# Optimization experiments

Hardware: AMD Instinct MI355X
Metric: run time of the kernel (lower is better)

## Reference

```python
import jax, jax.numpy as jnp
import numpy as np

BLOCK = (4, 8, 8)   # (t, h, w)
NH, D, DA = 8, 512, 64
EPS = 1e-5


def _layernorm(x, g, b):
    m = jnp.mean(x, axis=-1, keepdims=True)
    xc = x - m
    v = jnp.mean(xc * xc, axis=-1, keepdims=True)
    return xc * jax.lax.rsqrt(v + EPS) * g + b


def setup_inputs() -> dict:
    key = jax.random.key(0)
    ks = jax.random.split(key, 10)
    B, T, H, W = 2, 8, 32, 32
    t, h, w = BLOCK
    s_qkv = (2.0 / (D + DA)) ** 0.5   # xavier_normal for (d, da) fan
    s_lin = (2.0 / (D + D)) ** 0.5
    return {
        "x": jax.random.normal(ks[0], (B, D, T, H, W), jnp.float32),
        "dt_bank": 0.02 * jax.random.normal(ks[1], (NH, 2 * t - 1), jnp.float32),
        "dh_bank": 0.02 * jax.random.normal(ks[2], (NH, 2 * h - 1), jnp.float32),
        "dw_bank": 0.02 * jax.random.normal(ks[3], (NH, 2 * w - 1), jnp.float32),
        "ln1_g": jnp.ones((D,), jnp.float32),
        "ln1_b": jnp.zeros((D,), jnp.float32),
        "w_q": s_qkv * jax.random.normal(ks[4], (NH, D, DA), jnp.float32),
        "w_k": s_qkv * jax.random.normal(ks[5], (NH, D, DA), jnp.float32),
        "w_v": s_qkv * jax.random.normal(ks[6], (NH, D, DA), jnp.float32),
        "w_proj": s_lin * jax.random.normal(ks[7], (D, NH * DA), jnp.float32),
        "ln2_g": jnp.ones((D,), jnp.float32),
        "ln2_b": jnp.zeros((D,), jnp.float32),
        "w1": s_lin * jax.random.normal(ks[8], (D, D), jnp.float32),
        "b1": jnp.zeros((D,), jnp.float32),
        "w2": s_lin * jax.random.normal(ks[9], (D, D), jnp.float32),
        "b2": jnp.zeros((D,), jnp.float32),
    }


def _axial_bias(dt_bank, dh_bank, dw_bank):
    t, h, w = BLOCK
    thw = t * h * w
    ar = jnp.arange(thw)
    tt = ar // (h * w)
    hh = (ar // w) % h
    ww = ar % w
    # relative offsets shifted to be non-negative (matches dt += abs(dt.min()))
    it = tt[:, None] - tt[None, :] + (t - 1)
    ih = hh[:, None] - hh[None, :] + (h - 1)
    iw = ww[:, None] - ww[None, :] + (w - 1)
    return dt_bank[:, it] + dh_bank[:, ih] + dw_bank[:, iw]  # (NH, thw, thw)


def reference(x, dt_bank, dh_bank, dw_bank, ln1_g, ln1_b, w_q, w_k, w_v,
              w_proj, ln2_g, ln2_b, w1, b1, w2, b2):
    B, C, T, H, W = x.shape
    t, h, w = BLOCK
    st, sh, sw = T // t, H // h, W // w
    thw = t * h * w
    nb = B * st * sh * sw

    # block split: (B,C,T,H,W) -> (nb, thw, C)
    xb = x.reshape(B, C, st, t, sh, h, sw, w).transpose(0, 2, 4, 6, 1, 3, 5, 7)
    xb = xb.reshape(nb, C, thw).transpose(0, 2, 1)

    Bb = _axial_bias(dt_bank, dh_bank, dw_bank)  # (NH, thw, thw)

    # --- multi-head attention with additive axial bias ---
    resid = xb
    xn = _layernorm(xb, ln1_g, ln1_b)
    q = jnp.einsum('bnd,hde->hbne', xn, w_q)
    k = jnp.einsum('bnd,hde->hbne', xn, w_k)
    v = jnp.einsum('bnd,hde->hbne', xn, w_v)
    scale = 1.0 / jnp.sqrt(jnp.asarray(DA, x.dtype))
    attn = jnp.einsum('hbne,hbme->hbnm', q, k) * scale + Bb[:, None]
    attn = jax.nn.softmax(attn, axis=-1)
    out = jnp.einsum('hbnm,hbme->hbne', attn, v)         # (NH, nb, thw, DA)
    out = out.transpose(1, 2, 0, 3).reshape(nb, thw, NH * DA)  # head-major concat
    out = out @ w_proj.T + resid

    # --- FFN with residual ---
    y = _layernorm(out, ln2_g, ln2_b)
    y = jax.nn.relu(y @ w1.T + b1) @ w2.T + b2
    out = y + out

    # un-block: (nb, thw, C) -> (B,C,T,H,W)
    out = out.transpose(0, 2, 1).reshape(B, st, sh, sw, C, t, h, w)
    out = out.transpose(0, 4, 1, 5, 2, 6, 3, 7).reshape(B, C, T, H, W)
    return out
```

## Files before the change

kernel.cpp:

```cpp
#include <hip/hip_runtime.h>
#include <hip/hip_bf16.h>
#include <stdint.h>

typedef __attribute__((ext_vector_type(4))) float f32x4;
typedef __attribute__((ext_vector_type(8))) short s16x8;
typedef __attribute__((ext_vector_type(4))) short s16x4;
typedef __attribute__((ext_vector_type(8))) __bf16 b16x8;

__device__ __forceinline__ f32x4 mfma16(s16x8 a, s16x8 b, f32x4 c) {
  return __builtin_amdgcn_mfma_f32_16x16x32_bf16(
      __builtin_bit_cast(b16x8, a), __builtin_bit_cast(b16x8, b), c, 0, 0, 0);
}

__device__ __forceinline__ void gl_lds16(const void* g, void* l) {
  __builtin_amdgcn_global_load_lds(
      (const __attribute__((address_space(1))) void*)g,
      (__attribute__((address_space(3))) void*)l, 16, 0, 0);
}

__device__ __forceinline__ unsigned short f2bf(float f) {
  union { float f; unsigned u; } v; v.f = f;
  unsigned u = v.u;
  return (unsigned short)((u + 0x7FFFu + ((u >> 16) & 1u)) >> 16);
}

__global__ __launch_bounds__(256) void k_prep(
    const float* __restrict__ wq, const float* __restrict__ wk, const float* __restrict__ wv,
    const float* __restrict__ wp, const float* __restrict__ w1, const float* __restrict__ w2,
    unsigned short* __restrict__ qkvT, unsigned short* __restrict__ wpT,
    unsigned short* __restrict__ w1T, unsigned short* __restrict__ w2T)
{
  int i = blockIdx.x * 256 + threadIdx.x;
  if (i < 786432) {
    int n = i >> 9, d = i & 511;
    const float* src = (n < 512) ? wq : (n < 1024 ? wk : wv);
    int nn = n & 511;
    int h = nn >> 6, e = nn & 63;
    qkvT[i] = f2bf(src[((size_t)h * 512 + d) * 64 + e]);
  } else {
    int j = i - 786432;
    int w = j >> 18;
    int o = j & 262143;
    const float* s = (w == 0) ? wp : (w == 1 ? w1 : w2);
    unsigned short* dst = (w == 0) ? wpT : (w == 1 ? w1T : w2T);
    dst[o] = f2bf(s[o]);
  }
}

__global__ __launch_bounds__(256) void k_gather_ln(
    const float* __restrict__ x, const float* __restrict__ g1, const float* __restrict__ b1,
    float* __restrict__ xb, unsigned short* __restrict__ xn)
{
  __shared__ float lx[16][517];
  int gid = blockIdx.x;
  int h2 = gid & 1, hh = (gid >> 1) & 7, tt = (gid >> 4) & 3,
      shI = (gid >> 6) & 3, stI = (gid >> 8) & 1, bI = (gid >> 9) & 1;
  const float* xbase = x + (size_t)bI * 4194304 + (size_t)(stI * 4 + tt) * 1024
                       + (shI * 8 + hh) * 32 + h2 * 16;
  int t = threadIdx.x;
  for (int i = 0; i < 8; ++i) {
    int slot = i * 256 + t;
    int c = slot >> 2, w8 = slot & 3;
    const float4 v = *(const float4*)(xbase + (size_t)c * 8192 + w8 * 4);
    lx[w8 * 4 + 0][c] = v.x; lx[w8 * 4 + 1][c] = v.y;
    lx[w8 * 4 + 2][c] = v.z; lx[w8 * 4 + 3][c] = v.w;
  }
  __syncthreads();
  int lane = t & 63, wid = t >> 6;
  for (int q = 0; q < 4; ++q) {
    int widx = wid * 4 + q;
    float vv[8]; float s = 0.f, ss = 0.f;
    #pragma unroll
    for (int i = 0; i < 8; ++i) { float v = lx[widx][lane + i * 64]; vv[i] = v; s += v; ss += v * v; }
    #pragma unroll
    for (int d = 1; d < 64; d <<= 1) { s += __shfl_xor(s, d); ss += __shfl_xor(ss, d); }
    float mean = s * (1.f / 512.f);
    float var = ss * (1.f / 512.f) - mean * mean;
    float rs = rsqrtf(var + 1e-5f);
    int sw = h2 * 2 + (widx >> 3), ww = widx & 7;
    int blk = ((bI * 2 + stI) * 4 + shI) * 4 + sw;
    int n = tt * 64 + hh * 8 + ww;
    size_t base = ((size_t)blk * 256 + n) * 512;
    #pragma unroll
    for (int i = 0; i < 8; ++i) {
      int c = lane + i * 64;
      float v = vv[i];
      xb[base + c] = v;
      xn[base + c] = f2bf((v - mean) * rs * g1[c] + b1[c]);
    }
  }
}

template<int EPI>
__global__ __launch_bounds__(256, 2) void k_gemm(
    const unsigned short* __restrict__ A, const unsigned short* __restrict__ Bt,
    int M, int N,
    unsigned short* __restrict__ Cbf, float* __restrict__ Cf,
    const float* __restrict__ bias, const float* __restrict__ addf,
    unsigned short* __restrict__ vTout)
{
  constexpr int K = 512;
  __shared__ __align__(16) unsigned short a_lds[128 * 64];
  __shared__ __align__(16) unsigned short b_lds[128 * 64];
  int tid = threadIdx.x, lane = tid & 63, wid = tid >> 6;
  int m0 = blockIdx.x * 128, n0 = blockIdx.y * 128;
  int wm = (wid >> 1) * 64, wn = (wid & 1) * 64;
  int r15 = lane & 15, g = lane >> 4;

  f32x4 acc[4][4] = {};

  for (int ks = 0; ks < K; ks += 64) {
    #pragma unroll
    for (int s = 0; s < 4; ++s) {
      int seg = wid * 4 + s;
      int slot = seg * 64 + lane;
      int m = slot >> 3, lc = (slot & 7) ^ (m & 7);
      gl_lds16(A + (size_t)(m0 + m) * K + ks + lc * 8, (char*)a_lds + seg * 1024);
      gl_lds16(Bt + (size_t)(n0 + m) * K + ks + lc * 8, (char*)b_lds + seg * 1024);
    }
    __syncthreads();
    #pragma unroll
    for (int kk = 0; kk < 2; ++kk) {
      s16x8 af[4], bfr[4];
      #pragma unroll
      for (int f = 0; f < 4; ++f) {
        int mm = wm + f * 16 + r15;
        af[f] = *(const s16x8*)((const char*)a_lds + mm * 128 + (((kk * 4 + g) ^ (mm & 7)) * 16));
        int nn = wn + f * 16 + r15;
        bfr[f] = *(const s16x8*)((const char*)b_lds + nn * 128 + (((kk * 4 + g) ^ (nn & 7)) * 16));
      }
      #pragma unroll
      for (int fm = 0; fm < 4; ++fm)
        #pragma unroll
        for (int fn = 0; fn < 4; ++fn)
          acc[fm][fn] = mfma16(af[fm], bfr[fn], acc[fm][fn]);
    }
    __syncthreads();
  }

  int g4 = g * 4;
  #pragma unroll
  for (int fm = 0; fm < 4; ++fm) {
    #pragma unroll
    for (int fn = 0; fn < 4; ++fn) {
      int col = n0 + wn + fn * 16 + r15;
      int row0 = m0 + wm + fm * 16 + g4;
      if (EPI == 0 && col >= 1024) {
        int h = (col - 1024) >> 6, e = col & 63;
        int blk = row0 >> 8, mtok = row0 & 255;
        s16x4 pk;
        #pragma unroll
        for (int r = 0; r < 4; ++r) pk[r] = (short)f2bf(acc[fm][fn][r]);
        *(s16x4*)(vTout + (((size_t)blk * 8 + h) * 64 + e) * 256 + mtok) = pk;
      } else {
        #pragma unroll
        for (int r = 0; r < 4; ++r) {
          int row = row0 + r;
          float v = acc[fm][fn][r];
          if (EPI == 0) {
            Cbf[(size_t)row * 1536 + col] = f2bf(v);
          } else if (EPI == 1) {
            Cf[(size_t)row * 512 + col] = v + addf[(size_t)row * 512 + col];
          } else if (EPI == 2) {
            Cbf[(size_t)row * 512 + col] = f2bf(fmaxf(v + bias[col], 0.f));
          } else {
            Cf[(size_t)row * 512 + col] = v + bias[col] + addf[(size_t)row * 512 + col];
          }
        }
      }
    }
  }
}

__global__ __launch_bounds__(256, 2) void k_attn(
    const unsigned short* __restrict__ qkv, const unsigned short* __restrict__ vT,
    const float* __restrict__ dtb, const float* __restrict__ dhb, const float* __restrict__ dwb,
    unsigned short* __restrict__ aout)
{
  __shared__ __align__(16) unsigned short k_lds[64 * 64];
  __shared__ __align__(16) unsigned short v_lds[64 * 64];
  __shared__ __align__(16) unsigned short p_lds[4][64 * 64];
  __shared__ float bt_s[7], bh_s[15], bw_s[15];

  int tid = threadIdx.x, lane = tid & 63, wid = tid >> 6;
  int bk = blockIdx.x >> 3, h = blockIdx.x & 7;
  if (tid < 7) bt_s[tid] = dtb[h * 7 + tid];
  else if (tid < 22) bh_s[tid - 7] = dhb[h * 15 + tid - 7];
  else if (tid < 37) bw_s[tid - 22] = dwb[h * 15 + tid - 22];

  int r15 = lane & 15, g = lane >> 4;
  int wq0 = wid * 64;

  s16x8 qf[4][2];
  #pragma unroll
  for (int fn = 0; fn < 4; ++fn)
    #pragma unroll
    for (int kk = 0; kk < 2; ++kk)
      qf[fn][kk] = *(const s16x8*)(qkv + (size_t)(bk * 256 + wq0 + fn * 16 + r15) * 1536
                                   + h * 64 + kk * 32 + g * 8);

  f32x4 o[4][4] = {};
  float mrun[4] = {-1e30f, -1e30f, -1e30f, -1e30f};
  float lrun[4] = {0.f, 0.f, 0.f, 0.f};

  for (int mt = 0; mt < 4; ++mt) {
    int m0 = mt * 64;
    #pragma unroll
    for (int s = 0; s < 4; ++s) {
      int sg = wid * 4 + s;
      if (sg < 8) {
        int slot = sg * 64 + lane;
        int m = slot >> 3, lc = (slot & 7) ^ (m & 7);
        gl_lds16(qkv + (size_t)(bk * 256 + m0 + m) * 1536 + 512 + h * 64 + lc * 8,
                 (char*)k_lds + sg * 1024);
      } else {
        int slot = (sg - 8) * 64 + lane;
        int e = slot >> 3, lc = (slot & 7) ^ (e & 7);
        gl_lds16(vT + (((size_t)bk * 8 + h) * 64 + e) * 256 + m0 + lc * 8,
                 (char*)v_lds + (sg - 8) * 1024);
      }
    }
    __syncthreads();

    f32x4 st[4][4] = {};
    #pragma unroll
    for (int kk = 0; kk < 2; ++kk) {
      s16x8 kf[4];
      #pragma unroll
      for (int fm = 0; fm < 4; ++fm) {
        int m = fm * 16 + r15;
        kf[fm] = *(const s16x8*)((const char*)k_lds + m * 128 + (((kk * 4 + g) ^ (m & 7)) * 16));
      }
      #pragma unroll
      for (int fm = 0; fm < 4; ++fm)
        #pragma unroll
        for (int fn = 0; fn < 4; ++fn)
          st[fm][fn] = mfma16(kf[fm], qf[fn][kk], st[fm][fn]);
    }

    #pragma unroll
    for (int fn = 0; fn < 4; ++fn) {
      int n = wq0 + fn * 16 + r15;
      int ttn = n >> 6, hhn = (n >> 3) & 7, wwn = n & 7;
      float btc = bt_s[ttn - mt + 3];
      float bwv[4];
      #pragma unroll
      for (int r = 0; r < 4; ++r) bwv[r] = bw_s[wwn - (4 * (g & 1) + r) + 7];
      float vals[16];
      float mx = -1e30f;
      #pragma unroll
      for (int fm = 0; fm < 4; ++fm) {
        float bhv = bh_s[hhn - (fm * 2 + (g >> 1)) + 7];
        #pragma unroll
        for (int r = 0; r < 4; ++r) {
          float v = st[fm][fn][r] * 0.125f + btc + bhv + bwv[r];
          vals[fm * 4 + r] = v;
          mx = fmaxf(mx, v);
        }
      }
      mx = fmaxf(mx, __shfl_xor(mx, 16));
      mx = fmaxf(mx, __shfl_xor(mx, 32));
      float mnew = fmaxf(mrun[fn], mx);
      float alpha = __expf(mrun[fn] - mnew);
      mrun[fn] = mnew;
      float sum = 0.f;
      #pragma unroll
      for (int fm = 0; fm < 4; ++fm) {
        s16x4 pk;
        #pragma unroll
        for (int r = 0; r < 4; ++r) {
          float p = __expf(vals[fm * 4 + r] - mnew);
          sum += p;
          pk[r] = (short)f2bf(p);
        }
        int lc = fm * 2 + (g >> 1);
        int nl = fn * 16 + r15;
        *(s16x4*)((char*)(&p_lds[wid][0]) + nl * 128 + ((lc ^ (nl & 7)) * 16) + (g & 1) * 8) = pk;
      }
      sum += __shfl_xor(sum, 16);
      sum += __shfl_xor(sum, 32);
      lrun[fn] = lrun[fn] * alpha + sum;
      #pragma unroll
      for (int fe = 0; fe < 4; ++fe)
        #pragma unroll
        for (int r = 0; r < 4; ++r)
          o[fe][fn][r] *= alpha;
    }
    asm volatile("s_waitcnt lgkmcnt(0)" ::: "memory");

    #pragma unroll
    for (int mm = 0; mm < 2; ++mm) {
      s16x8 vf[4], pf[4];
      #pragma unroll
      for (int fe = 0; fe < 4; ++fe) {
        int e = fe * 16 + r15;
        vf[fe] = *(const s16x8*)((const char*)v_lds + e * 128 + (((mm * 4 + g) ^ (e & 7)) * 16));
      }
      #pragma unroll
      for (int fn = 0; fn < 4; ++fn) {
        int nl = fn * 16 + r15;
        pf[fn] = *(const s16x8*)((const char*)(&p_lds[wid][0]) + nl * 128 + (((mm * 4 + g) ^ (nl & 7)) * 16));
      }
      #pragma unroll
      for (int fe = 0; fe < 4; ++fe)
        #pragma unroll
        for (int fn = 0; fn < 4; ++fn)
          o[fe][fn] = mfma16(vf[fe], pf[fn], o[fe][fn]);
    }
    __syncthreads();
  }

  #pragma unroll
  for (int fn = 0; fn < 4; ++fn) {
    float inv = 1.f / lrun[fn];
    #pragma unroll
    for (int fe = 0; fe < 4; ++fe)
      #pragma unroll
      for (int r = 0; r < 4; ++r)
        o[fe][fn][r] *= inv;
  }
  #pragma unroll
  for (int fe = 0; fe < 4; ++fe) {
    int lc = fe * 2 + (g >> 1);
    #pragma unroll
    for (int fn = 0; fn < 4; ++fn) {
      int nl = fn * 16 + r15;
      s16x4 pk;
      #pragma unroll
      for (int r = 0; r < 4; ++r) pk[r] = (short)f2bf(o[fe][fn][r]);
      *(s16x4*)((char*)(&p_lds[wid][0]) + nl * 128 + ((lc ^ (nl & 7)) * 16) + (g & 1) * 8) = pk;
    }
  }
  asm volatile("s_waitcnt lgkmcnt(0)" ::: "memory");
  #pragma unroll
  for (int it = 0; it < 8; ++it) {
    int nl = it * 8 + (lane >> 3);
    int lc = lane & 7;
    s16x8 v = *(const s16x8*)((const char*)(&p_lds[wid][0]) + nl * 128 + ((lc ^ (nl & 7)) * 16));
    *(s16x8*)(aout + (size_t)(bk * 256 + wq0 + nl) * 512 + h * 64 + lc * 8) = v;
  }
}

__global__ __launch_bounds__(256) void k_ln2(
    const float* __restrict__ in, const float* __restrict__ g2, const float* __restrict__ b2,
    unsigned short* __restrict__ out)
{
  int token = blockIdx.x * 4 + (threadIdx.x >> 6);
  int lane = threadIdx.x & 63;
  const float* row = in + (size_t)token * 512;
  float vv[8]; float s = 0.f, ss = 0.f;
  #pragma unroll
  for (int i = 0; i < 8; ++i) { float v = row[lane + i * 64]; vv[i] = v; s += v; ss += v * v; }
  #pragma unroll
  for (int d = 1; d < 64; d <<= 1) { s += __shfl_xor(s, d); ss += __shfl_xor(ss, d); }
  float mean = s * (1.f / 512.f);
  float var = ss * (1.f / 512.f) - mean * mean;
  float rs = rsqrtf(var + 1e-5f);
  #pragma unroll
  for (int i = 0; i < 8; ++i) {
    int c = lane + i * 64;
    out[(size_t)token * 512 + c] = f2bf((vv[i] - mean) * rs * g2[c] + b2[c]);
  }
}

__global__ __launch_bounds__(64) void k_scatter(
    const float* __restrict__ fin, float* __restrict__ out)
{
  __shared__ float lx[32][33];
  int gid = blockIdx.x;
  int cc = gid & 15;
  int sg = gid >> 4;
  int hh = sg & 7, tt = (sg >> 3) & 3, shI = (sg >> 5) & 3, stI = (sg >> 7) & 1, bI = (sg >> 8) & 1;
  int c0 = cc * 32;
  int l = threadIdx.x;
  #pragma unroll
  for (int i = 0; i < 4; ++i) {
    int slot = i * 64 + l;
    int tok = slot >> 3, c4 = slot & 7;
    int blk = ((bI * 2 + stI) * 4 + shI) * 4 + (tok >> 3);
    int n = tt * 64 + hh * 8 + (tok & 7);
    const float4 v = *(const float4*)(fin + ((size_t)blk * 256 + n) * 512 + c0 + c4 * 4);
    lx[tok][c4 * 4 + 0] = v.x; lx[tok][c4 * 4 + 1] = v.y;
    lx[tok][c4 * 4 + 2] = v.z; lx[tok][c4 * 4 + 3] = v.w;
  }
  __syncthreads();
  size_t obase = (size_t)bI * 4194304 + (size_t)(stI * 4 + tt) * 1024 + (shI * 8 + hh) * 32;
  #pragma unroll
  for (int i = 0; i < 4; ++i) {
    int crow = i * 8 + (l >> 3), w4 = l & 7;
    float4 v;
    v.x = lx[w4 * 4 + 0][crow]; v.y = lx[w4 * 4 + 1][crow];
    v.z = lx[w4 * 4 + 2][crow]; v.w = lx[w4 * 4 + 3][crow];
    *(float4*)(out + obase + (size_t)(c0 + crow) * 8192 + w4 * 4) = v;
  }
}

extern "C" void kernel_launch(void* const* d_in, const int* in_sizes, int n_in,
                              void* d_out, int out_size, void* d_ws, size_t ws_size,
                              hipStream_t stream)
{
  const float* x   = (const float*)d_in[0];
  const float* dtb = (const float*)d_in[1];
  const float* dhb = (const float*)d_in[2];
  const float* dwb = (const float*)d_in[3];
  const float* g1  = (const float*)d_in[4];
  const float* bb1 = (const float*)d_in[5];
  const float* wq  = (const float*)d_in[6];
  const float* wk  = (const float*)d_in[7];
  const float* wv  = (const float*)d_in[8];
  const float* wp  = (const float*)d_in[9];
  const float* g2  = (const float*)d_in[10];
  const float* bb2 = (const float*)d_in[11];
  const float* w1  = (const float*)d_in[12];
  const float* fb1 = (const float*)d_in[13];
  const float* w2  = (const float*)d_in[14];
  const float* fb2 = (const float*)d_in[15];

  char* ws = (char*)d_ws;
  float*          xb   = (float*)(ws + 0);
  unsigned short* vT   = (unsigned short*)(ws + 33554432);
  float*          out1 = (float*)(ws + 33554432);
  unsigned short* qkv  = (unsigned short*)(ws + 67108864);
  unsigned short* xn   = (unsigned short*)(ws + 117440512);
  unsigned short* qkvT = (unsigned short*)(ws + 134217728);
  unsigned short* wpT  = (unsigned short*)(ws + 135790592);
  unsigned short* w1T  = (unsigned short*)(ws + 136314880);
  unsigned short* w2T  = (unsigned short*)(ws + 136839168);

  unsigned short* attn_out = xn;
  unsigned short* yb = xn;
  unsigned short* h1 = qkv;
  float* finalb = xb;
  float* outp = (float*)d_out;

  k_prep<<<6144, 256, 0, stream>>>(wq, wk, wv, wp, w1, w2, qkvT, wpT, w1T, w2T);
  k_gather_ln<<<1024, 256, 0, stream>>>(x, g1, bb1, xb, xn);
  k_gemm<0><<<dim3(128, 12), 256, 0, stream>>>(xn, qkvT, 16384, 1536, qkv, nullptr, nullptr, nullptr, vT);
  k_attn<<<512, 256, 0, stream>>>(qkv, vT, dtb, dhb, dwb, attn_out);
  k_gemm<1><<<dim3(128, 4), 256, 0, stream>>>(attn_out, wpT, 16384, 512, nullptr, out1, nullptr, xb, nullptr);
  k_ln2<<<4096, 256, 0, stream>>>(out1, g2, bb2, yb);
  k_gemm<2><<<dim3(128, 4), 256, 0, stream>>>(yb, w1T, 16384, 512, h1, nullptr, fb1, nullptr, nullptr);
  k_gemm<3><<<dim3(128, 4), 256, 0, stream>>>(h1, w2T, 16384, 512, nullptr, finalb, fb2, out1, nullptr);
  k_scatter<<<8192, 64, 0, stream>>>(finalb, outp);
}
```

Before: 180.7 us.

## Rework attention softmax, store residual in bf16, swizzle GEMM grid, vectorize LN2

The attention kernel now loads K and V fragments straight from global memory into registers, with no LDS staging and no block-level barriers. It folds the scale and bias into base-2 exponentials, precomputes the per-lane axial bias values, and skips rescaling of the running maximum unless it grows by more than a threshold. The intermediate residual out1 is stored in bf16 instead of fp32, which halves its traffic in the projection, LN2 and second FFN GEMM, at some cost in precision. The GEMMs get a workgroup index swizzle for cache locality and setprio around the MFMA loops, and LN2 switches to vectorized 16-byte loads and stores.

```diff
diff --git a/kernel.cpp b/kernel.cpp
--- a/kernel.cpp
+++ b/kernel.cpp
@@ -23,6 +23,22 @@
   unsigned u = v.u;
   return (unsigned short)((u + 0x7FFFu + ((u >> 16) & 1u)) >> 16);
 }
+
+__device__ __forceinline__ float bf2f(unsigned short u) {
+  union { unsigned u; float f; } v; v.u = ((unsigned)u) << 16; return v.f;
+}
+
+__device__ __forceinline__ unsigned cvt_pk_bf16(float a, float b) {
+  unsigned r;
+  asm("v_cvt_pk_bf16_f32 %0, %1, %2" : "=v"(r) : "v"(a), "v"(b));
+  return r;
+}
+
+#if __has_builtin(__builtin_amdgcn_exp2f)
+#define EXP2F(x) __builtin_amdgcn_exp2f(x)
+#else
+#define EXP2F(x) exp2f(x)
+#endif
 
 __global__ __launch_bounds__(256) void k_prep(
     const float* __restrict__ wq, const float* __restrict__ wk, const float* __restrict__ wv,
@@ -97,13 +113,18 @@
     int M, int N,
     unsigned short* __restrict__ Cbf, float* __restrict__ Cf,
     const float* __restrict__ bias, const float* __restrict__ addf,
+    const unsigned short* __restrict__ addbf,
     unsigned short* __restrict__ vTout)
 {
   constexpr int K = 512;
   __shared__ __align__(16) unsigned short a_lds[128 * 64];
   __shared__ __align__(16) unsigned short b_lds[128 * 64];
   int tid = threadIdx.x, lane = tid & 63, wid = tid >> 6;
-  int m0 = blockIdx.x * 128, n0 = blockIdx.y * 128;
+  int nwg = gridDim.x * gridDim.y;
+  int lin = blockIdx.y * gridDim.x + blockIdx.x;
+  int swz = (lin & 7) * (nwg >> 3) + (lin >> 3);
+  int bx = swz % gridDim.x, by = swz / gridDim.x;
+  int m0 = bx * 128, n0 = by * 128;
   int wm = (wid >> 1) * 64, wn = (wid & 1) * 64;
   int r15 = lane & 15, g = lane >> 4;
 
@@ -129,11 +150,13 @@
         int nn = wn + f * 16 + r15;
         bfr[f] = *(const s16x8*)((const char*)b_lds + nn * 128 + (((kk * 4 + g) ^ (nn & 7)) * 16));
       }
+      __builtin_amdgcn_s_setprio(1);
       #pragma unroll
       for (int fm = 0; fm < 4; ++fm)
         #pragma unroll
         for (int fn = 0; fn < 4; ++fn)
           acc[fm][fn] = mfma16(af[fm], bfr[fn], acc[fm][fn]);
+      __builtin_amdgcn_s_setprio(0);
     }
     __syncthreads();
   }
@@ -160,11 +183,11 @@
           if (EPI == 0) {
             Cbf[(size_t)row * 1536 + col] = f2bf(v);
           } else if (EPI == 1) {
-            Cf[(size_t)row * 512 + col] = v + addf[(size_t)row * 512 + col];
+            Cbf[(size_t)row * 512 + col] = f2bf(v + addf[(size_t)row * 512 + col]);
           } else if (EPI == 2) {
             Cbf[(size_t)row * 512 + col] = f2bf(fmaxf(v + bias[col], 0.f));
           } else {
-            Cf[(size_t)row * 512 + col] = v + bias[col] + addf[(size_t)row * 512 + col];
+            Cf[(size_t)row * 512 + col] = v + bias[col] + bf2f(addbf[(size_t)row * 512 + col]);
           }
         }
       }
@@ -177,190 +200,184 @@
     const float* __restrict__ dtb, const float* __restrict__ dhb, const float* __restrict__ dwb,
     unsigned short* __restrict__ aout)
 {
-  __shared__ __align__(16) unsigned short k_lds[64 * 64];
-  __shared__ __align__(16) unsigned short v_lds[64 * 64];
   __shared__ __align__(16) unsigned short p_lds[4][64 * 64];
-  __shared__ float bt_s[7], bh_s[15], bw_s[15];
+  __shared__ float bt_s[8], bh_s[16], bw_s[16];
+
+  const float L2E = 1.44269504f;
+  const float SC = 0.125f * 1.44269504f;
 
   int tid = threadIdx.x, lane = tid & 63, wid = tid >> 6;
   int bk = blockIdx.x >> 3, h = blockIdx.x & 7;
-  if (tid < 7) bt_s[tid] = dtb[h * 7 + tid];
-  else if (tid < 22) bh_s[tid - 7] = dhb[h * 15 + tid - 7];
-  else if (tid < 37) bw_s[tid - 22] = dwb[h * 15 + tid - 22];
+  if (tid < 7) bt_s[tid] = dtb[h * 7 + tid] * L2E;
+  else if (tid < 22) bh_s[tid - 7] = dhb[h * 15 + tid - 7] * L2E;
+  else if (tid < 37) bw_s[tid - 22] = dwb[h * 15 + tid - 22] * L2E;
 
   int r15 = lane & 15, g = lane >> 4;
   int wq0 = wid * 64;
+  size_t bkBase = (size_t)bk * 256;
 
   s16x8 qf[4][2];
   #pragma unroll
   for (int fn = 0; fn < 4; ++fn)
     #pragma unroll
     for (int kk = 0; kk < 2; ++kk)
-      qf[fn][kk] = *(const s16x8*)(qkv + (size_t)(bk * 256 + wq0 + fn * 16 + r15) * 1536
+      qf[fn][kk] = *(const s16x8*)(qkv + (bkBase + wq0 + fn * 16 + r15) * 1536
                                    + h * 64 + kk * 32 + g * 8);
+
+  __syncthreads();
+
+  float btoff[4], hb[7], wb[4];
+  {
+    int Dh = (r15 >> 3) - (g >> 1) + 7;
+    int Wb = (r15 & 7) - 4 * (g & 1) + 7;
+    #pragma unroll
+    for (int mt = 0; mt < 4; ++mt) btoff[mt] = bt_s[wid + 3 - mt];
+    #pragma unroll
+    for (int d = 0; d < 7; ++d) hb[d] = bh_s[Dh + 2 * d - 6];
+    #pragma unroll
+    for (int r = 0; r < 4; ++r) wb[r] = bw_s[Wb - r];
+  }
 
   f32x4 o[4][4] = {};
   float mrun[4] = {-1e30f, -1e30f, -1e30f, -1e30f};
   float lrun[4] = {0.f, 0.f, 0.f, 0.f};
-
+  char* p_w = (char*)(&p_lds[wid][0]);
+
+  #pragma unroll
   for (int mt = 0; mt < 4; ++mt) {
     int m0 = mt * 64;
-    #pragma unroll
-    for (int s = 0; s < 4; ++s) {
-      int sg = wid * 4 + s;
-      if (sg < 8) {
-        int slot = sg * 64 + lane;
-        int m = slot >> 3, lc = (slot & 7) ^ (m & 7);
-        gl_lds16(qkv + (size_t)(bk * 256 + m0 + m) * 1536 + 512 + h * 64 + lc * 8,
-                 (char*)k_lds + sg * 1024);
-      } else {
-        int slot = (sg - 8) * 64 + lane;
-        int e = slot >> 3, lc = (slot & 7) ^ (e & 7);
-        gl_lds16(vT + (((size_t)bk * 8 + h) * 64 + e) * 256 + m0 + lc * 8,
-                 (char*)v_lds + (sg - 8) * 1024);
-      }
-    }
-    __syncthreads();
+
+    s16x8 vf[4][2];
+    #pragma unroll
+    for (int fe = 0; fe < 4; ++fe)
+      #pragma unroll
+      for (int mm = 0; mm < 2; ++mm)
+        vf[fe][mm] = *(const s16x8*)(vT + (((size_t)bk * 8 + h) * 64 + fe * 16 + r15) * 256
+                                     + m0 + mm * 32 + g * 8);
 
     f32x4 st[4][4] = {};
     #pragma unroll
     for (int kk = 0; kk < 2; ++kk) {
       s16x8 kf[4];
       #pragma unroll
-      for (int fm = 0; fm < 4; ++fm) {
-        int m = fm * 16 + r15;
-        kf[fm] = *(const s16x8*)((const char*)k_lds + m * 128 + (((kk * 4 + g) ^ (m & 7)) * 16));
-      }
+      for (int fm = 0; fm < 4; ++fm)
+        kf[fm] = *(const s16x8*)(qkv + (bkBase + m0 + fm * 16 + r15) * 1536
+                                 + 512 + h * 64 + kk * 32 + g * 8);
+      __builtin_amdgcn_s_setprio(1);
       #pragma unroll
       for (int fm = 0; fm < 4; ++fm)
         #pragma unroll
         for (int fn = 0; fn < 4; ++fn)
           st[fm][fn] = mfma16(kf[fm], qf[fn][kk], st[fm][fn]);
+      __builtin_amdgcn_s_setprio(0);
     }
 
     #pragma unroll
     for (int fn = 0; fn < 4; ++fn) {
-      int n = wq0 + fn * 16 + r15;
-      int ttn = n >> 6, hhn = (n >> 3) & 7, wwn = n & 7;
-      float btc = bt_s[ttn - mt + 3];
-      float bwv[4];
-      #pragma unroll
-      for (int r = 0; r < 4; ++r) bwv[r] = bw_s[wwn - (4 * (g & 1) + r) + 7];
       float vals[16];
       float mx = -1e30f;
       #pragma unroll
       for (int fm = 0; fm < 4; ++fm) {
-        float bhv = bh_s[hhn - (fm * 2 + (g >> 1)) + 7];
+        float cc = btoff[mt] + hb[fn - fm + 3];
         #pragma unroll
         for (int r = 0; r < 4; ++r) {
-          float v = st[fm][fn][r] * 0.125f + btc + bhv + bwv[r];
+          float v = fmaf(st[fm][fn][r], SC, cc) + wb[r];
           vals[fm * 4 + r] = v;
           mx = fmaxf(mx, v);
         }
       }
       mx = fmaxf(mx, __shfl_xor(mx, 16));
       mx = fmaxf(mx, __shfl_xor(mx, 32));
-      float mnew = fmaxf(mrun[fn], mx);
-      float alpha = __expf(mrun[fn] - mnew);
-      mrun[fn] = mnew;
-      float sum = 0.f;
-      #pragma unroll
-      for (int fm = 0; fm < 4; ++fm) {
-        s16x4 pk;
-        #pragma unroll
-        for (int r = 0; r < 4; ++r) {
-          float p = __expf(vals[fm * 4 + r] - mnew);
-          sum += p;
-          pk[r] = (short)f2bf(p);
-        }
-        int lc = fm * 2 + (g >> 1);
-        int nl = fn * 16 + r15;
-        *(s16x4*)((char*)(&p_lds[wid][0]) + nl * 128 + ((lc ^ (nl & 7)) * 16) + (g & 1) * 8) = pk;
-      }
+      if (!__all(mx <= mrun[fn] + 8.f)) {
+        float mnew = fmaxf(mrun[fn], mx);
+        float al = EXP2F(mrun[fn] - mnew);
+        mrun[fn] = mnew;
+        lrun[fn] *= al;
+        #pragma unroll
+        for (int fe = 0; fe < 4; ++fe)
+          #pragma unroll
+          for (int r = 0; r < 4; ++r)
+            o[fe][fn][r] *= al;
+      }
+      float m_c = mrun[fn];
+      float p[16]; float sum = 0.f;
+      #pragma unroll
+      for (int i = 0; i < 16; ++i) { p[i] = EXP2F(vals[i] - m_c); sum += p[i]; }
       sum += __shfl_xor(sum, 16);
       sum += __shfl_xor(sum, 32);
-      lrun[fn] = lrun[fn] * alpha + sum;
-      #pragma unroll
-      for (int fe = 0; fe < 4; ++fe)
-        #pragma unroll
-        for (int r = 0; r < 4; ++r)
-          o[fe][fn][r] *= alpha;
+      lrun[fn] += sum;
+      int nl = fn * 16 + r15;
+      char* prow = p_w + nl * 128 + (g & 1) * 8;
+      #pragma unroll
+      for (int fm = 0; fm < 4; ++fm) {
+        unsigned u0 = cvt_pk_bf16(p[fm * 4 + 0], p[fm * 4 + 1]);
+        unsigned u1 = cvt_pk_bf16(p[fm * 4 + 2], p[fm * 4 + 3]);
+        int lc = fm * 2 + (g >> 1);
+        *(uint2*)(prow + ((lc ^ (nl & 7)) * 16)) = make_uint2(u0, u1);
+      }
     }
     asm volatile("s_waitcnt lgkmcnt(0)" ::: "memory");
+    __builtin_amdgcn_sched_barrier(0);
 
     #pragma unroll
     for (int mm = 0; mm < 2; ++mm) {
-      s16x8 vf[4], pf[4];
-      #pragma unroll
-      for (int fe = 0; fe < 4; ++fe) {
-        int e = fe * 16 + r15;
-        vf[fe] = *(const s16x8*)((const char*)v_lds + e * 128 + (((mm * 4 + g) ^ (e & 7)) * 16));
-      }
+      s16x8 pf[4];
       #pragma unroll
       for (int fn = 0; fn < 4; ++fn) {
         int nl = fn * 16 + r15;
-        pf[fn] = *(const s16x8*)((const char*)(&p_lds[wid][0]) + nl * 128 + (((mm * 4 + g) ^ (nl & 7)) * 16));
-      }
+        pf[fn] = *(const s16x8*)(p_w + nl * 128 + (((mm * 4 + g) ^ (nl & 7)) * 16));
+      }
+      __builtin_amdgcn_s_setprio(1);
       #pragma unroll
       for (int fe = 0; fe < 4; ++fe)
         #pragma unroll
         for (int fn = 0; fn < 4; ++fn)
-          o[fe][fn] = mfma16(vf[fe], pf[fn], o[fe][fn]);
-    }
-    __syncthreads();
+          o[fe][fn] = mfma16(vf[fe][mm], pf[fn], o[fe][fn]);
+      __builtin_amdgcn_s_setprio(0);
+    }
   }
 
   #pragma unroll
   for (int fn = 0; fn < 4; ++fn) {
     float inv = 1.f / lrun[fn];
-    #pragma unroll
-    for (int fe = 0; fe < 4; ++fe)
-      #pragma unroll
-      for (int r = 0; r < 4; ++r)
-        o[fe][fn][r] *= inv;
-  }
-  #pragma unroll
-  for (int fe = 0; fe < 4; ++fe) {
-    int lc = fe * 2 + (g >> 1);
-    #pragma unroll
-    for (int fn = 0; fn < 4; ++fn) {
-      int nl = fn * 16 + r15;
-      s16x4 pk;
-      #pragma unroll
-      for (int r = 0; r < 4; ++r) pk[r] = (short)f2bf(o[fe][fn][r]);
-      *(s16x4*)((char*)(&p_lds[wid][0]) + nl * 128 + ((lc ^ (nl & 7)) * 16) + (g & 1) * 8) = pk;
-    }
-  }
-  asm volatile("s_waitcnt lgkmcnt(0)" ::: "memory");
-  #pragma unroll
-  for (int it = 0; it < 8; ++it) {
-    int nl = it * 8 + (lane >> 3);
-    int lc = lane & 7;
-    s16x8 v = *(const s16x8*)((const char*)(&p_lds[wid][0]) + nl * 128 + ((lc ^ (nl & 7)) * 16));
-    *(s16x8*)(aout + (size_t)(bk * 256 + wq0 + nl) * 512 + h * 64 + lc * 8) = v;
+    size_t rowb = (bkBase + wq0 + fn * 16 + r15) * 512 + h * 64;
+    #pragma unroll
+    for (int fe = 0; fe < 4; ++fe) {
+      unsigned u0 = cvt_pk_bf16(o[fe][fn][0] * inv, o[fe][fn][1] * inv);
+      unsigned u1 = cvt_pk_bf16(o[fe][fn][2] * inv, o[fe][fn][3] * inv);
+      *(uint2*)(aout + rowb + fe * 16 + g * 4) = make_uint2(u0, u1);
+    }
   }
 }
 
 __global__ __launch_bounds__(256) void k_ln2(
-    const float* __restrict__ in, const float* __restrict__ g2, const float* __restrict__ b2,
+    const unsigned short* __restrict__ in, const float* __restrict__ g2, const float* __restrict__ b2,
     unsigned short* __restrict__ out)
 {
   int token = blockIdx.x * 4 + (threadIdx.x >> 6);
   int lane = threadIdx.x & 63;
-  const float* row = in + (size_t)token * 512;
+  s16x8 v8 = *(const s16x8*)(in + (size_t)token * 512 + lane * 8);
   float vv[8]; float s = 0.f, ss = 0.f;
   #pragma unroll
-  for (int i = 0; i < 8; ++i) { float v = row[lane + i * 64]; vv[i] = v; s += v; ss += v * v; }
+  for (int i = 0; i < 8; ++i) {
+    float v = bf2f((unsigned short)v8[i]); vv[i] = v; s += v; ss += v * v;
+  }
   #pragma unroll
   for (int d = 1; d < 64; d <<= 1) { s += __shfl_xor(s, d); ss += __shfl_xor(ss, d); }
   float mean = s * (1.f / 512.f);
   float var = ss * (1.f / 512.f) - mean * mean;
   float rs = rsqrtf(var + 1e-5f);
-  #pragma unroll
-  for (int i = 0; i < 8; ++i) {
-    int c = lane + i * 64;
-    out[(size_t)token * 512 + c] = f2bf((vv[i] - mean) * rs * g2[c] + b2[c]);
-  }
+  const float4 gA = *(const float4*)(g2 + lane * 8);
+  const float4 gB = *(const float4*)(g2 + lane * 8 + 4);
+  const float4 bA = *(const float4*)(b2 + lane * 8);
+  const float4 bB = *(const float4*)(b2 + lane * 8 + 4);
+  float gv[8] = {gA.x, gA.y, gA.z, gA.w, gB.x, gB.y, gB.z, gB.w};
+  float bv[8] = {bA.x, bA.y, bA.z, bA.w, bB.x, bB.y, bB.z, bB.w};
+  s16x8 o8;
+  #pragma unroll
+  for (int i = 0; i < 8; ++i)
+    o8[i] = (short)f2bf((vv[i] - mean) * rs * gv[i] + bv[i]);
+  *(s16x8*)(out + (size_t)token * 512 + lane * 8) = o8;
 }
 
 __global__ __launch_bounds__(64) void k_scatter(
@@ -419,7 +436,7 @@
   char* ws = (char*)d_ws;
   float*          xb   = (float*)(ws + 0);
   unsigned short* vT   = (unsigned short*)(ws + 33554432);
-  float*          out1 = (float*)(ws + 33554432);
+  unsigned short* out1b= (unsigned short*)(ws + 33554432);
   unsigned short* qkv  = (unsigned short*)(ws + 67108864);
   unsigned short* xn   = (unsigned short*)(ws + 117440512);
   unsigned short* qkvT = (unsigned short*)(ws + 134217728);
@@ -435,11 +452,11 @@
 
   k_prep<<<6144, 256, 0, stream>>>(wq, wk, wv, wp, w1, w2, qkvT, wpT, w1T, w2T);
   k_gather_ln<<<1024, 256, 0, stream>>>(x, g1, bb1, xb, xn);
-  k_gemm<0><<<dim3(128, 12), 256, 0, stream>>>(xn, qkvT, 16384, 1536, qkv, nullptr, nullptr, nullptr, vT);
+  k_gemm<0><<<dim3(128, 12), 256, 0, stream>>>(xn, qkvT, 16384, 1536, qkv, nullptr, nullptr, nullptr, nullptr, vT);
   k_attn<<<512, 256, 0, stream>>>(qkv, vT, dtb, dhb, dwb, attn_out);
-  k_gemm<1><<<dim3(128, 4), 256, 0, stream>>>(attn_out, wpT, 16384, 512, nullptr, out1, nullptr, xb, nullptr);
-  k_ln2<<<4096, 256, 0, stream>>>(out1, g2, bb2, yb);
-  k_gemm<2><<<dim3(128, 4), 256, 0, stream>>>(yb, w1T, 16384, 512, h1, nullptr, fb1, nullptr, nullptr);
-  k_gemm<3><<<dim3(128, 4), 256, 0, stream>>>(h1, w2T, 16384, 512, nullptr, finalb, fb2, out1, nullptr);
+  k_gemm<1><<<dim3(128, 4), 256, 0, stream>>>(attn_out, wpT, 16384, 512, out1b, nullptr, nullptr, xb, nullptr, nullptr);
+  k_ln2<<<4096, 256, 0, stream>>>(out1b, g2, bb2, yb);
+  k_gemm<2><<<dim3(128, 4), 256, 0, stream>>>(yb, w1T, 16384, 512, h1, nullptr, fb1, nullptr, nullptr, nullptr);
+  k_gemm<3><<<dim3(128, 4), 256, 0, stream>>>(h1, w2T, 16384, 512, nullptr, finalb, fb2, nullptr, out1b, nullptr);
   k_scatter<<<8192, 64, 0, stream>>>(finalb, outp);
 }
```

After: 178.1 us. About the same (-1.5%).
